# Optimization experiments

Hardware: AMD Instinct MI355X
Metric: run time of the kernel (lower is better)

The kernel has to match this reference:

```python
import jax, jax.numpy as jnp
import numpy as np

S = 8            # n_internal_streams
N = 2**S - 1     # 255 cliques (all non-empty subsets of streams)
D = 32           # half_dim = consciousness_dim // 2
INPUT_DIM = 512
NUM_ITER = 5
B = 1024


def _configs():
    # binary membership of each clique (non-empty subsets), [N, S]
    return ((np.arange(1, 2**S)[:, None] >> np.arange(S)) & 1).astype(np.float32)


def setup_inputs() -> dict:
    key = jax.random.key(0)
    ks = jax.random.split(key, 10)
    cfg = _configs()
    depths = cfg.sum(-1)
    # topological amplitude init: gaussian profile over clique depth
    center, sigma = S / 2.0, S / 3.0
    prof = np.exp(-((depths - center) ** 2) / (2 * sigma ** 2))
    prof = prof / (np.linalg.norm(prof) + 1e-8)
    psi_A0 = jnp.asarray(np.broadcast_to(prof[None, :, None], (1, N, D)).copy(),
                         jnp.float32) + jax.random.normal(ks[0], (1, N, D)) * 0.01
    inp = {
        'network_state': jax.random.normal(ks[1], (B, INPUT_DIM), jnp.float32),
        'W_streams': jax.random.normal(ks[2], (S * D, INPUT_DIM)) / np.sqrt(INPUT_DIM),
        'b_streams': jnp.zeros((S * D,), jnp.float32),
        'W_A': jax.random.normal(ks[3], (D, D)) / np.sqrt(D),
        'b_A': jnp.zeros((D,), jnp.float32),
        'W_phi': jax.random.normal(ks[4], (D, D)) / np.sqrt(D),
        'b_phi': jnp.zeros((D,), jnp.float32),
        'psi_A0': psi_A0,
        'psi_phi0': jax.random.normal(ks[5], (1, N, D)) * 0.3,
        'W_comp': jax.random.normal(ks[6], (32, N)) / np.sqrt(N),
        'b_comp': jnp.zeros((32,), jnp.float32),
        'W_read': jax.random.normal(ks[7], (2 * D, 32 * D)) / np.sqrt(32 * D),
        'b_read': jnp.zeros((2 * D,), jnp.float32),
        'alpha_kin': jnp.asarray(0.5, jnp.float32),
        'mass_sq': jnp.asarray(0.1, jnp.float32),
        'potential_weight': jnp.asarray(0.3, jnp.float32),
        'input_weight': jnp.asarray(0.5, jnp.float32),
        'evolution_rate': jnp.asarray(0.3, jnp.float32),
        'phase_coupling': jnp.asarray(1.0, jnp.float32),
    }
    return inp


def reference(network_state, W_streams, b_streams, W_A, b_A, W_phi, b_phi,
              psi_A0, psi_phi0, W_comp, b_comp, W_read, b_read,
              alpha_kin, mass_sq, potential_weight, input_weight,
              evolution_rate, phase_coupling):
    cfg = jnp.asarray(_configs())                      # [N,S]
    depths = cfg.sum(-1)                               # [N]
    # Hamming-distance kernel between clique configurations
    Ham = cfg @ (1.0 - cfg).T + (1.0 - cfg) @ cfg.T    # [N,N]
    K = jnp.exp(-Ham / S)
    krow = K.sum(1)                                    # [N]

    Bb = network_state.shape[0]
    feats = (network_state @ W_streams.T + b_streams).reshape(Bb, S, D)
    # clique features: mean of member-stream features
    cf = jnp.einsum('ns,bsd->bnd', cfg, feats) / depths[None, :, None]
    A_input = jax.nn.softplus(cf @ W_A.T + b_A)        # [B,N,D]
    phi_input = jnp.pi * jnp.tanh(cf @ W_phi.T + b_phi)

    A = jax.nn.softplus(jnp.broadcast_to(psi_A0, (Bb, N, D)))
    phi = jnp.broadcast_to(psi_phi0, (Bb, N, D))
    dt = jax.nn.sigmoid(evolution_rate)

    for _ in range(NUM_ITER):
        # laplacian: sum_j K_ij (A_j - A_i) / N  (factorized, same math)
        KA = jnp.einsum('ij,bjd->bid', K, A)
        lap = (KA - krow[None, :, None] * A) / N
        sp, cp = jnp.sin(phi), jnp.cos(phi)
        Ks = jnp.einsum('ij,bjd->bid', K, sp)
        Kc = jnp.einsum('ij,bjd->bid', K, cp)
        # sum_j K_ij A_i sin(phi_j - phi_i) / N
        pc = A * (cp * Ks - sp * Kc) / N
        # nonlocal potential: V_i = sum_j K_ij A_j cos(phi_j - phi_i) / N
        KAc = jnp.einsum('ij,bjd->bid', K, A * cp)
        KAs = jnp.einsum('ij,bjd->bid', K, A * sp)
        V = (cp * KAc + sp * KAs) / N
        input_drive = A_input * jnp.sin(phi_input - phi)
        dA = (alpha_kin * lap + potential_weight * V - mass_sq * A
              + input_weight * (A_input - A))
        A = jax.nn.softplus(A + dt * dA)               # updated A used in dphi
        dphi = alpha_kin * pc / (A + 1e-8) + input_weight * input_drive
        phi = phi + dt * dphi
        # per-clique norm clip to 1
        norms = jnp.maximum(jnp.linalg.norm(A, axis=-1, keepdims=True), 1e-8)
        A = A * jnp.where(norms > 1.0, 1.0 / norms, 1.0)

    A_t = jnp.swapaxes(A, 1, 2)                        # [B,D,N]
    Ac = jax.nn.relu(A_t @ W_comp.T + b_comp)          # [B,D,32]
    ro = Ac.reshape(Bb, -1) @ W_read.T + b_read        # [B,2D]
    amplitude = jax.nn.softplus(ro[:, :D])
    phase = jnp.tanh(ro[:, D:] * phase_coupling) * jnp.pi
    psi = (amplitude * jnp.cos(phase)).astype(jnp.complex64) + 1j * (amplitude * jnp.sin(phase)).astype(jnp.complex64)
    return psi, amplitude, phase
```

## Files before the change

kernel.cpp:

```cpp
#include <hip/hip_runtime.h>
#include <math.h>

#define PI_F   3.14159265358979f
#define QF     0.88249690258459546f
#define INV255 (1.0f/255.0f)

__device__ __forceinline__ float softplus_f(float x){
    return fmaxf(x, 0.0f) + __logf(1.0f + __expf(-fabsf(x)));
}
__device__ __forceinline__ float tanh_fast(float x){
    const float e = __expf(2.0f*x);
    return fmaf(-2.0f, __builtin_amdgcn_rcpf(e + 1.0f), 1.0f);
}

template<int CTRL>
__device__ __forceinline__ float dppmov(float x){
    return __int_as_float(__builtin_amdgcn_mov_dpp(__float_as_int(x), CTRL, 0xF, 0xF, false));
}
__device__ __forceinline__ float lxor1 (float x){ return dppmov<0xB1>(x);  }
__device__ __forceinline__ float lxor2 (float x){ return dppmov<0x4E>(x);  }
__device__ __forceinline__ float lxor8 (float x){ return dppmov<0x128>(x); }
__device__ __forceinline__ float lxor4 (float x){ return __int_as_float(__builtin_amdgcn_ds_swizzle(__float_as_int(x), 0x101F)); }
__device__ __forceinline__ float lxor16(float x){ return __int_as_float(__builtin_amdgcn_ds_swizzle(__float_as_int(x), 0x401F)); }
__device__ __forceinline__ float lxor32(float x){ return __shfl_xor(x, 32, 64); }

template<int CTRL>
__device__ __forceinline__ float dppadd(float v){
    return v + __int_as_float(__builtin_amdgcn_update_dpp(0, __float_as_int(v), CTRL, 0xF, 0xF, true));
}
__device__ __forceinline__ float wave_sum63(float v){
    v = dppadd<0x111>(v);
    v = dppadd<0x112>(v);
    v = dppadd<0x114>(v);
    v = dppadd<0x118>(v);
    v = dppadd<0x142>(v);
    v = dppadd<0x143>(v);
    return v;
}

template<int NA>
__device__ __forceinline__ void bflyN(float (&x)[NA][4]){
    const float qv = QF;
    #pragma unroll
    for (int a = 0; a < NA; a++){
        #pragma unroll
        for (int r = 0; r < 4; r++) x[a][r] = fmaf(lxor1 (x[a][r]), qv, x[a][r]);
    }
    #pragma unroll
    for (int a = 0; a < NA; a++){
        #pragma unroll
        for (int r = 0; r < 4; r++) x[a][r] = fmaf(lxor2 (x[a][r]), qv, x[a][r]);
    }
    #pragma unroll
    for (int a = 0; a < NA; a++){
        #pragma unroll
        for (int r = 0; r < 4; r++) x[a][r] = fmaf(lxor8 (x[a][r]), qv, x[a][r]);
    }
    #pragma unroll
    for (int a = 0; a < NA; a++){
        #pragma unroll
        for (int r = 0; r < 4; r++) x[a][r] = fmaf(lxor4 (x[a][r]), qv, x[a][r]);
    }
    #pragma unroll
    for (int a = 0; a < NA; a++){
        #pragma unroll
        for (int r = 0; r < 4; r++) x[a][r] = fmaf(lxor16(x[a][r]), qv, x[a][r]);
    }
    #pragma unroll
    for (int a = 0; a < NA; a++){
        #pragma unroll
        for (int r = 0; r < 4; r++) x[a][r] = fmaf(lxor32(x[a][r]), qv, x[a][r]);
    }
    #pragma unroll
    for (int a = 0; a < NA; a++){
        float t0 = x[a][0], t2 = x[a][2];
        x[a][0] = fmaf(QF, x[a][1], x[a][0]);
        x[a][1] = fmaf(QF, t0,      x[a][1]);
        x[a][2] = fmaf(QF, x[a][3], x[a][2]);
        x[a][3] = fmaf(QF, t2,      x[a][3]);
        t0 = x[a][0]; float t1 = x[a][1];
        x[a][0] = fmaf(QF, x[a][2], x[a][0]);
        x[a][1] = fmaf(QF, x[a][3], x[a][1]);
        x[a][2] = fmaf(QF, t0,      x[a][2]);
        x[a][3] = fmaf(QF, t1,      x[a][3]);
    }
}

__global__ __launch_bounds__(256) void prep_kernel(
        const float* __restrict__ Ws,    const float* __restrict__ psiA0,
        const float* __restrict__ psiP0, float* __restrict__ WsT,
        float* __restrict__ psiA0T,      float* __restrict__ psiP0T)
{
    if (blockIdx.x < 32){
        __shared__ float tile[64][65];
        const int rt = blockIdx.x & 3, ct = blockIdx.x >> 2;
        const int r0 = rt*64, c0 = ct*64;
        const int tx = threadIdx.x & 63, ty = threadIdx.x >> 6;
        #pragma unroll
        for (int k = 0; k < 16; k++){
            const int row = ty*16 + k;
            tile[row][tx] = Ws[(r0+row)*512 + c0 + tx];
        }
        __syncthreads();
        #pragma unroll
        for (int k = 0; k < 16; k++){
            const int row = ty*16 + k;
            WsT[(c0+row)*256 + r0 + tx] = tile[tx][row];
        }
    } else {
        const int d = blockIdx.x - 32;
        const int n = threadIdx.x;
        const float a = (n > 0) ? psiA0[(n-1)*32 + d] : 0.0f;
        const float p = (n > 0) ? psiP0[(n-1)*32 + d] : 0.0f;
        psiA0T[d*256 + n] = a;
        psiP0T[d*256 + n] = p;
    }
}

template<bool USET>
__global__ __launch_bounds__(256) void fused_kernel(
        const float* __restrict__ ns,
        const float* __restrict__ Ws,
        const float* __restrict__ WsT,
        const float* __restrict__ bs,
        const float* __restrict__ WA,
        const float* __restrict__ bA,
        const float* __restrict__ WP,
        const float* __restrict__ bP,
        const float* __restrict__ psiA0,
        const float* __restrict__ psiP0,
        const float* __restrict__ psiA0T,
        const float* __restrict__ psiP0T,
        const float* __restrict__ Wcomp,
        const float* __restrict__ bcomp,
        const float* __restrict__ Wread,
        const float* __restrict__ bread,
        const float* __restrict__ p_alpha, const float* __restrict__ p_msq,
        const float* __restrict__ p_pw,    const float* __restrict__ p_iw,
        const float* __restrict__ p_evo,   const float* __restrict__ p_pcpl,
        float* __restrict__ out, int Bb)
{
    __shared__ __align__(16) float nsb[512];
    __shared__ __align__(16) float fe[256];
    __shared__ __align__(16) float hA[256];
    __shared__ __align__(16) float hP[256];
    __shared__ __align__(16) float red[2][1024];
    __shared__ __align__(16) float ac[1024];
    __shared__ __align__(16) float rop[256];

    const int b   = blockIdx.x;
    const int tid = threadIdx.x;
    const int w   = tid >> 6, l = tid & 63;

    const float alpha = p_alpha[0], msq = p_msq[0], pw = p_pw[0], iw = p_iw[0];
    const float pcpl  = p_pcpl[0];
    const float dt    = 1.0f / (1.0f + __expf(-p_evo[0]));
    const float dta  = dt * alpha * INV255;
    const float dtpw = dt * pw * INV255;
    const float c0   = 1.0f - dt * (msq + iw);
    const float dtiw = dt * iw;

    nsb[tid]       = ns[b*512 + tid];
    nsb[tid + 256] = ns[b*512 + 256 + tid];
    __syncthreads();
    if (USET){
        float f = bs[tid];
        const float4* nb4 = (const float4*)nsb;
        #pragma unroll 8
        for (int j4 = 0; j4 < 128; j4++){
            const float4 nv = nb4[j4];
            const float* col = WsT + j4*1024 + tid;
            f = fmaf(col[0],   nv.x, f);
            f = fmaf(col[256], nv.y, f);
            f = fmaf(col[512], nv.z, f);
            f = fmaf(col[768], nv.w, f);
        }
        fe[tid] = f;
    } else {
        float f = bs[tid];
        const float4* wr  = (const float4*)(Ws + tid*512);
        const float4* nb4 = (const float4*)nsb;
        #pragma unroll 8
        for (int i = 0; i < 128; i++){
            const float4 wv = wr[i], nv = nb4[i];
            f = fmaf(wv.x, nv.x, f); f = fmaf(wv.y, nv.y, f);
            f = fmaf(wv.z, nv.z, f); f = fmaf(wv.w, nv.w, f);
        }
        fe[tid] = f;
    }
    __syncthreads();
    {
        const int s = tid >> 5, d = tid & 31;
        float a = 0.0f, p = 0.0f;
        #pragma unroll 8
        for (int dp = 0; dp < 32; dp++){
            const float fv = fe[s*32 + dp];
            a = fmaf(WA[d*32 + dp], fv, a);
            p = fmaf(WP[d*32 + dp], fv, p);
        }
        hA[tid] = a; hP[tid] = p;
    }
    __syncthreads();

    int   nn[4];
    float krow[4], rdep[4];
    const float m0 = (l == 0) ? 0.0f : 1.0f;
    float c18;
    { const float t1 = 1.0f + QF, t2 = t1*t1, t4 = t2*t2; c18 = t4*t4; }
    #pragma unroll
    for (int r = 0; r < 4; r++){
        nn[r] = l + 64*r;
        const int pop = __popc(nn[r]);
        krow[r]  = c18 - __expf(-0.125f * (float)pop);
        rdep[r]  = 1.0f / (float)(pop ? pop : 1);
    }

    float A[8][4], phi[8][4], CAp[8][4], Dsp[8][4], Dcp[8][4];

    #pragma unroll
    for (int dd = 0; dd < 8; dd++){
        const int d = w*8 + dd;
        const float bAd = bA[d], bPd = bP[d];
        float gA_[8], gP_[8];
        #pragma unroll
        for (int s = 0; s < 8; s++){ gA_[s] = hA[s*32 + d]; gP_[s] = hP[s*32 + d]; }
        #pragma unroll
        for (int r = 0; r < 4; r++){
            float sA = 0.0f, sP = 0.0f;
            #pragma unroll
            for (int s = 0; s < 8; s++){
                if ((nn[r] >> s) & 1){ sA += gA_[s]; sP += gP_[s]; }
            }
            const float uA  = fmaf(sA, rdep[r], bAd);
            const float uP  = fmaf(sP, rdep[r], bPd);
            const float Ain = softplus_f(uA);
            const float pin = PI_F * tanh_fast(uP);
            const float si = __sinf(pin), ci = __cosf(pin);
            const float ca = dtiw * Ain;
            CAp[dd][r] = ca; Dsp[dd][r] = ca * si; Dcp[dd][r] = ca * ci;
            if (USET){
                A[dd][r]   = softplus_f(psiA0T[d*256 + nn[r]]);
                phi[dd][r] = psiP0T[d*256 + nn[r]];
            } else {
                const int nm1 = (nn[r] > 0) ? (nn[r] - 1) : 0;
                A[dd][r]   = softplus_f(psiA0[nm1*32 + d]);
                phi[dd][r] = psiP0[nm1*32 + d];
            }
        }
    }

    for (int it = 0; it < 4; it++){
        const int pbuf = it & 1;
        float nrm[4] = {0.f, 0.f, 0.f, 0.f};
        #pragma unroll
        for (int dd = 0; dd < 8; dd++){
            float sp[4], cp[4];
            float x[5][4];
            {
                sp[0] = __sinf(phi[dd][0]); cp[0] = __cosf(phi[dd][0]);
                const float xa = A[dd][0] * m0;
                x[0][0] = xa;
                x[1][0] = sp[0] * m0;
                x[2][0] = cp[0] * m0;
                x[3][0] = xa * cp[0];
                x[4][0] = xa * sp[0];
            }
            #pragma unroll
            for (int r = 1; r < 4; r++){
                sp[r] = __sinf(phi[dd][r]); cp[r] = __cosf(phi[dd][r]);
                const float xa = A[dd][r];
                x[0][r] = xa;
                x[1][r] = sp[r];
                x[2][r] = cp[r];
                x[3][r] = xa * cp[r];
                x[4][r] = xa * sp[r];
            }
            bflyN<5>(x);
            #pragma unroll
            for (int r = 0; r < 4; r++){
                const float Ao   = A[dd][r];
                const float lapp = fmaf(-krow[r], Ao, x[0][r]);
                const float Vp   = fmaf(cp[r], x[3][r], sp[r]*x[4][r]);
                float Aarg = fmaf(c0, Ao, CAp[dd][r]);
                Aarg = fmaf(dta,  lapp, Aarg);
                Aarg = fmaf(dtpw, Vp,   Aarg);
                const float An = softplus_f(Aarg);
                const float Pp = fmaf(-sp[r], x[2][r], cp[r]*x[1][r]);
                const float rr = __builtin_amdgcn_rcpf(An + 1e-8f);
                float pb = fmaf(Dsp[dd][r], cp[r], phi[dd][r]);
                pb = fmaf(-Dcp[dd][r], sp[r], pb);
                phi[dd][r] = fmaf(dta*Ao, Pp*rr, pb);
                A[dd][r]   = An;
                nrm[r]     = fmaf(An, An, nrm[r]);
            }
        }
        #pragma unroll
        for (int r = 0; r < 4; r++) red[pbuf][w*256 + nn[r]] = nrm[r];
        __syncthreads();
        float scl[4];
        #pragma unroll
        for (int r = 0; r < 4; r++){
            const float t = red[pbuf][nn[r]] + red[pbuf][256 + nn[r]]
                          + red[pbuf][512 + nn[r]] + red[pbuf][768 + nn[r]];
            scl[r] = (t > 1.0f) ? rsqrtf(t) : 1.0f;
        }
        #pragma unroll
        for (int dd = 0; dd < 8; dd++)
            #pragma unroll
            for (int r = 0; r < 4; r++) A[dd][r] *= scl[r];
    }

    {
        float nrm[4] = {0.f, 0.f, 0.f, 0.f};
        #pragma unroll
        for (int dd = 0; dd < 8; dd++){
            float sp[4], cp[4];
            float y[3][4];
            {
                sp[0] = __sinf(phi[dd][0]); cp[0] = __cosf(phi[dd][0]);
                const float xa = A[dd][0] * m0;
                y[0][0] = xa;
                y[1][0] = xa * cp[0];
                y[2][0] = xa * sp[0];
            }
            #pragma unroll
            for (int r = 1; r < 4; r++){
                sp[r] = __sinf(phi[dd][r]); cp[r] = __cosf(phi[dd][r]);
                const float xa = A[dd][r];
                y[0][r] = xa;
                y[1][r] = xa * cp[r];
                y[2][r] = xa * sp[r];
            }
            bflyN<3>(y);
            #pragma unroll
            for (int r = 0; r < 4; r++){
                const float Ao   = A[dd][r];
                const float lapp = fmaf(-krow[r], Ao, y[0][r]);
                const float Vp   = fmaf(cp[r], y[1][r], sp[r]*y[2][r]);
                float Aarg = fmaf(c0, Ao, CAp[dd][r]);
                Aarg = fmaf(dta,  lapp, Aarg);
                Aarg = fmaf(dtpw, Vp,   Aarg);
                const float An = softplus_f(Aarg);
                A[dd][r]   = An;
                nrm[r]     = fmaf(An, An, nrm[r]);
            }
        }
        #pragma unroll
        for (int r = 0; r < 4; r++) red[0][w*256 + nn[r]] = nrm[r];
        __syncthreads();
        float scl[4];
        #pragma unroll
        for (int r = 0; r < 4; r++){
            const float t = red[0][nn[r]] + red[0][256 + nn[r]]
                          + red[0][512 + nn[r]] + red[0][768 + nn[r]];
            scl[r] = (t > 1.0f) ? rsqrtf(t) : 1.0f;
        }
        #pragma unroll
        for (int dd = 0; dd < 8; dd++)
            #pragma unroll
            for (int r = 0; r < 4; r++) A[dd][r] *= scl[r];
    }

    #pragma unroll
    for (int dd = 0; dd < 8; dd++) A[dd][0] *= m0;

    for (int c = 0; c < 32; c++){
        float wv[4];
        #pragma unroll
        for (int r = 0; r < 4; r++){
            const int idx = c*255 + nn[r] - 1;
            wv[r] = Wcomp[idx < 0 ? 0 : idx];
        }
        const float bc = bcomp[c];
        #pragma unroll
        for (int dd = 0; dd < 8; dd++){
            float v = wv[0] * A[dd][0];
            v = fmaf(wv[1], A[dd][1], v);
            v = fmaf(wv[2], A[dd][2], v);
            v = fmaf(wv[3], A[dd][3], v);
            v = wave_sum63(v);
            if (l == 63)
                ac[(w*8 + dd)*32 + c] = fmaxf(v + bc, 0.0f);
        }
    }
    __syncthreads();

    {
        const int k = tid >> 2, part = tid & 3;
        const float4* Wr4 = (const float4*)Wread + k*256;
        const float4* ac4 = (const float4*)ac;
        float s = 0.0f;
        #pragma unroll 4
        for (int jj = 0; jj < 64; jj++){
            const int j4 = part + 4*jj;
            const float4 wv = Wr4[j4];
            const float4 av = ac4[j4];
            s = fmaf(wv.x, av.x, s); s = fmaf(wv.y, av.y, s);
            s = fmaf(wv.z, av.z, s); s = fmaf(wv.w, av.w, s);
        }
        rop[tid] = s;
    }
    __syncthreads();
    if (tid < 32){
        const float ra = rop[tid*4] + rop[tid*4+1] + rop[tid*4+2] + rop[tid*4+3] + bread[tid];
        const int   t2 = tid + 32;
        const float rp = rop[t2*4] + rop[t2*4+1] + rop[t2*4+2] + rop[t2*4+3] + bread[t2];
        const float amp = softplus_f(ra);
        const float ph  = PI_F * tanhf(rp * pcpl);
        const float cph = __cosf(ph);
        const int o = b*32 + tid;
        out[o]         = amp * cph;
        out[Bb*32 + o] = amp;
        out[Bb*64 + o] = ph;
    }
}

extern "C" void kernel_launch(void* const* d_in, const int* in_sizes, int n_in,
                              void* d_out, int out_size, void* d_ws, size_t ws_size,
                              hipStream_t stream) {
    const float* ns      = (const float*)d_in[0];
    const float* Ws      = (const float*)d_in[1];
    const float* bs      = (const float*)d_in[2];
    const float* WA      = (const float*)d_in[3];
    const float* bA      = (const float*)d_in[4];
    const float* WP      = (const float*)d_in[5];
    const float* bP      = (const float*)d_in[6];
    const float* psiA0   = (const float*)d_in[7];
    const float* psiP0   = (const float*)d_in[8];
    const float* Wcomp   = (const float*)d_in[9];
    const float* bcomp   = (const float*)d_in[10];
    const float* Wread   = (const float*)d_in[11];
    const float* bread   = (const float*)d_in[12];
    const float* p_alpha = (const float*)d_in[13];
    const float* p_msq   = (const float*)d_in[14];
    const float* p_pw    = (const float*)d_in[15];
    const float* p_iw    = (const float*)d_in[16];
    const float* p_evo   = (const float*)d_in[17];
    const float* p_pcpl  = (const float*)d_in[18];

    const int Bb = in_sizes[0] / 512;

    const size_t need = (size_t)(512*256 + 2*32*256) * sizeof(float);
    if (ws_size >= need){
        float* WsT    = (float*)d_ws;
        float* psiA0T = WsT + 512*256;
        float* psiP0T = psiA0T + 32*256;
        prep_kernel<<<64, 256, 0, stream>>>(Ws, psiA0, psiP0, WsT, psiA0T, psiP0T);
        fused_kernel<true><<<Bb, 256, 0, stream>>>(ns, Ws, WsT, bs, WA, bA, WP, bP,
                                                   psiA0, psiP0, psiA0T, psiP0T,
                                                   Wcomp, bcomp, Wread, bread,
                                                   p_alpha, p_msq, p_pw, p_iw,
                                                   p_evo, p_pcpl, (float*)d_out, Bb);
    } else {
        fused_kernel<false><<<Bb, 256, 0, stream>>>(ns, Ws, nullptr, bs, WA, bA, WP, bP,
                                                    psiA0, psiP0, nullptr, nullptr,
                                                    Wcomp, bcomp, Wread, bread,
                                                    p_alpha, p_msq, p_pw, p_iw,
                                                    p_evo, p_pcpl, (float*)d_out, Bb);
    }
}
```

Measured before the change: 321.3 us.

## Precompute batch-independent first evolution step in prep kernel

The initial psi state is the same for every sample, so the Laplacian, potential and phase-coupling terms of the first iteration are computed once in the prep kernel. Their sin/cos values are stored in workspace. The per-sample kernel only adds the input-drive terms, applies softplus and the norm clip, then runs one fewer full iteration. This removes about a quarter of the per-sample butterfly and trig work, at the cost of extra workspace reads and one more block barrier.

```diff
diff --git a/kernel.cpp b/kernel.cpp
--- a/kernel.cpp
+++ b/kernel.cpp
@@ -88,32 +88,82 @@
 
 __global__ __launch_bounds__(256) void prep_kernel(
         const float* __restrict__ Ws,    const float* __restrict__ psiA0,
-        const float* __restrict__ psiP0, float* __restrict__ WsT,
-        float* __restrict__ psiA0T,      float* __restrict__ psiP0T)
+        const float* __restrict__ psiP0, const float* __restrict__ p_alpha,
+        const float* __restrict__ p_msq, const float* __restrict__ p_pw,
+        const float* __restrict__ p_iw,  const float* __restrict__ p_evo,
+        float* __restrict__ WsT,  float* __restrict__ Xc,  float* __restrict__ P0c,
+        float* __restrict__ S0c,  float* __restrict__ C0c, float* __restrict__ F0c)
 {
     if (blockIdx.x < 32){
         __shared__ float tile[64][65];
         const int rt = blockIdx.x & 3, ct = blockIdx.x >> 2;
-        const int r0 = rt*64, c0 = ct*64;
+        const int r0 = rt*64, c0t = ct*64;
         const int tx = threadIdx.x & 63, ty = threadIdx.x >> 6;
         #pragma unroll
         for (int k = 0; k < 16; k++){
             const int row = ty*16 + k;
-            tile[row][tx] = Ws[(r0+row)*512 + c0 + tx];
+            tile[row][tx] = Ws[(r0+row)*512 + c0t + tx];
         }
         __syncthreads();
         #pragma unroll
         for (int k = 0; k < 16; k++){
             const int row = ty*16 + k;
-            WsT[(c0+row)*256 + r0 + tx] = tile[tx][row];
-        }
-    } else {
-        const int d = blockIdx.x - 32;
-        const int n = threadIdx.x;
-        const float a = (n > 0) ? psiA0[(n-1)*32 + d] : 0.0f;
-        const float p = (n > 0) ? psiP0[(n-1)*32 + d] : 0.0f;
-        psiA0T[d*256 + n] = a;
-        psiP0T[d*256 + n] = p;
+            WsT[(c0t+row)*256 + r0 + tx] = tile[tx][row];
+        }
+        return;
+    }
+    const int tid = threadIdx.x;
+    const int w = tid >> 6, l = tid & 63;
+    const float alpha = p_alpha[0], msq = p_msq[0], pw = p_pw[0], iw = p_iw[0];
+    const float dt   = 1.0f / (1.0f + __expf(-p_evo[0]));
+    const float dta  = dt * alpha * INV255;
+    const float dtpw = dt * pw * INV255;
+    const float c0   = 1.0f - dt * (msq + iw);
+    const float m0 = (l == 0) ? 0.0f : 1.0f;
+    int nn[4]; float krow[4];
+    float c18;
+    { const float t1 = 1.0f + QF, t2 = t1*t1, t4 = t2*t2; c18 = t4*t4; }
+    #pragma unroll
+    for (int r = 0; r < 4; r++){
+        nn[r] = l + 64*r;
+        krow[r] = c18 - __expf(-0.125f * (float)__popc(nn[r]));
+    }
+    #pragma unroll
+    for (int dd = 0; dd < 8; dd++){
+        const int d = w*8 + dd;
+        float A0[4], ph0[4], sp[4], cp[4];
+        float x[5][4];
+        #pragma unroll
+        for (int r = 0; r < 4; r++){
+            const int n = nn[r];
+            A0[r]  = (n > 0) ? softplus_f(psiA0[(n-1)*32 + d]) : 0.0f;
+            ph0[r] = (n > 0) ? psiP0[(n-1)*32 + d] : 0.0f;
+            sp[r] = __sinf(ph0[r]); cp[r] = __cosf(ph0[r]);
+            const float mk = (r == 0) ? m0 : 1.0f;
+            const float xa = A0[r] * mk;
+            x[0][r] = xa;
+            x[1][r] = sp[r] * mk;
+            x[2][r] = cp[r] * mk;
+            x[3][r] = xa * cp[r];
+            x[4][r] = xa * sp[r];
+        }
+        bflyN<5>(x);
+        #pragma unroll
+        for (int r = 0; r < 4; r++){
+            const float Ao   = A0[r];
+            const float lapp = fmaf(-krow[r], Ao, x[0][r]);
+            const float Vp   = fmaf(cp[r], x[3][r], sp[r]*x[4][r]);
+            const float Pp   = fmaf(-sp[r], x[2][r], cp[r]*x[1][r]);
+            float X = c0 * Ao;
+            X = fmaf(dta,  lapp, X);
+            X = fmaf(dtpw, Vp,   X);
+            const int idx = d*256 + nn[r];
+            Xc[idx]  = X;
+            P0c[idx] = dta * Ao * Pp;
+            S0c[idx] = sp[r];
+            C0c[idx] = cp[r];
+            F0c[idx] = ph0[r];
+        }
     }
 }
 
@@ -129,8 +179,11 @@
         const float* __restrict__ bP,
         const float* __restrict__ psiA0,
         const float* __restrict__ psiP0,
-        const float* __restrict__ psiA0T,
-        const float* __restrict__ psiP0T,
+        const float* __restrict__ Xc,
+        const float* __restrict__ P0c,
+        const float* __restrict__ S0c,
+        const float* __restrict__ C0c,
+        const float* __restrict__ F0c,
         const float* __restrict__ Wcomp,
         const float* __restrict__ bcomp,
         const float* __restrict__ Wread,
@@ -216,6 +269,7 @@
     }
 
     float A[8][4], phi[8][4], CAp[8][4], Dsp[8][4], Dcp[8][4];
+    float nrm0[4] = {0.f, 0.f, 0.f, 0.f};
 
     #pragma unroll
     for (int dd = 0; dd < 8; dd++){
@@ -239,8 +293,14 @@
             const float ca = dtiw * Ain;
             CAp[dd][r] = ca; Dsp[dd][r] = ca * si; Dcp[dd][r] = ca * ci;
             if (USET){
-                A[dd][r]   = softplus_f(psiA0T[d*256 + nn[r]]);
-                phi[dd][r] = psiP0T[d*256 + nn[r]];
+                const int idx = d*256 + nn[r];
+                const float An = softplus_f(Xc[idx] + ca);
+                const float rr = __builtin_amdgcn_rcpf(An + 1e-8f);
+                float pb = fmaf(Dsp[dd][r], C0c[idx], F0c[idx]);
+                pb = fmaf(-Dcp[dd][r], S0c[idx], pb);
+                phi[dd][r] = fmaf(P0c[idx], rr, pb);
+                A[dd][r]   = An;
+                nrm0[r]    = fmaf(An, An, nrm0[r]);
             } else {
                 const int nm1 = (nn[r] > 0) ? (nn[r] - 1) : 0;
                 A[dd][r]   = softplus_f(psiA0[nm1*32 + d]);
@@ -249,8 +309,26 @@
         }
     }
 
-    for (int it = 0; it < 4; it++){
-        const int pbuf = it & 1;
+    if (USET){
+        #pragma unroll
+        for (int r = 0; r < 4; r++) red[0][w*256 + nn[r]] = nrm0[r];
+        __syncthreads();
+        float scl[4];
+        #pragma unroll
+        for (int r = 0; r < 4; r++){
+            const float t = red[0][nn[r]] + red[0][256 + nn[r]]
+                          + red[0][512 + nn[r]] + red[0][768 + nn[r]];
+            scl[r] = (t > 1.0f) ? rsqrtf(t) : 1.0f;
+        }
+        #pragma unroll
+        for (int dd = 0; dd < 8; dd++)
+            #pragma unroll
+            for (int r = 0; r < 4; r++) A[dd][r] *= scl[r];
+    }
+
+    const int NFULL = USET ? 3 : 4;
+    for (int it = 0; it < NFULL; it++){
+        const int pbuf = USET ? ((it + 1) & 1) : (it & 1);
         float nrm[4] = {0.f, 0.f, 0.f, 0.f};
         #pragma unroll
         for (int dd = 0; dd < 8; dd++){
@@ -440,20 +518,26 @@
 
     const int Bb = in_sizes[0] / 512;
 
-    const size_t need = (size_t)(512*256 + 2*32*256) * sizeof(float);
+    const size_t need = (size_t)(512*256 + 5*32*256) * sizeof(float);
     if (ws_size >= need){
-        float* WsT    = (float*)d_ws;
-        float* psiA0T = WsT + 512*256;
-        float* psiP0T = psiA0T + 32*256;
-        prep_kernel<<<64, 256, 0, stream>>>(Ws, psiA0, psiP0, WsT, psiA0T, psiP0T);
+        float* WsT = (float*)d_ws;
+        float* Xc  = WsT + 512*256;
+        float* P0c = Xc  + 32*256;
+        float* S0c = P0c + 32*256;
+        float* C0c = S0c + 32*256;
+        float* F0c = C0c + 32*256;
+        prep_kernel<<<33, 256, 0, stream>>>(Ws, psiA0, psiP0,
+                                            p_alpha, p_msq, p_pw, p_iw, p_evo,
+                                            WsT, Xc, P0c, S0c, C0c, F0c);
         fused_kernel<true><<<Bb, 256, 0, stream>>>(ns, Ws, WsT, bs, WA, bA, WP, bP,
-                                                   psiA0, psiP0, psiA0T, psiP0T,
+                                                   psiA0, psiP0, Xc, P0c, S0c, C0c, F0c,
                                                    Wcomp, bcomp, Wread, bread,
                                                    p_alpha, p_msq, p_pw, p_iw,
                                                    p_evo, p_pcpl, (float*)d_out, Bb);
     } else {
         fused_kernel<false><<<Bb, 256, 0, stream>>>(ns, Ws, nullptr, bs, WA, bA, WP, bP,
-                                                    psiA0, psiP0, nullptr, nullptr,
+                                                    psiA0, psiP0,
+                                                    nullptr, nullptr, nullptr, nullptr, nullptr,
                                                     Wcomp, bcomp, Wread, bread,
                                                     p_alpha, p_msq, p_pw, p_iw,
                                                     p_evo, p_pcpl, (float*)d_out, Bb);
```

After: 309.6 us (median of 2 runs). -3.6%, faster.
